# Optimization experiments

Measured on AMD Instinct MI355X. Metric: run time of the kernel, lower is better.

Reference implementation:

```python
import jax, jax.numpy as jnp
import numpy as np

HEADS = 16
KEY = 64          # key_size == size_per_head
NEG = 1e10


def setup_inputs() -> dict:
    key = jax.random.key(0)
    k1, k2, k3, k4, k5, k6 = jax.random.split(key, 6)
    B, S, D = 2, 2048, 1024
    scale = 1.0 / np.sqrt(D).astype(np.float32)
    return {
        "q": jax.random.normal(k1, (B, S, D), jnp.float32),
        "k": jax.random.normal(k2, (B, S, D), jnp.float32),
        "v": jax.random.normal(k3, (B, S, D), jnp.float32),
        "Wq": jax.random.normal(k4, (D, HEADS * KEY), jnp.float32) * scale,
        "Wk": jax.random.normal(k5, (D, HEADS * KEY), jnp.float32) * scale,
        "Wv": jax.random.normal(k6, (D, HEADS * KEY), jnp.float32) * scale,
    }


def reference(q, k, v, Wq, Wk, Wv):
    B, Sq, _ = q.shape
    Skv = k.shape[1]
    # projections (no bias), split heads: (B, S, H*Dh) -> (B, H, S, Dh)
    qw = (q @ Wq).reshape(B, Sq, HEADS, KEY).transpose(0, 2, 1, 3)
    kw = (k @ Wk).reshape(B, Skv, HEADS, KEY).transpose(0, 2, 1, 3)
    vw = (v @ Wv).reshape(B, Skv, HEADS, KEY).transpose(0, 2, 1, 3)
    inv_sqrt_d = jnp.asarray(1.0 / np.sqrt(KEY), dtype=qw.dtype)
    a = jnp.einsum("bhqd,bhkd->bhqk", qw, kw) * inv_sqrt_d  # (B,H,Sq,Skv)
    # mask_right=True: causal additive mask a - (1 - tril)*1e10
    causal = jnp.tril(jnp.ones((Sq, Skv), dtype=a.dtype))
    a = a - (1.0 - causal) * jnp.asarray(NEG, dtype=a.dtype)
    a = jax.nn.softmax(a, axis=-1)
    o = jnp.einsum("bhqk,bhkd->bhqd", a, vw)  # (B,H,Sq,Dh)
    o = o.transpose(0, 2, 1, 3).reshape(B, Sq, HEADS * KEY)
    return o
```

## Files before the change

kernel.cpp:

```cpp
#include <hip/hip_runtime.h>
#include <hip/hip_bf16.h>

#define HEADS 16
#define KEY   64
#define BB    2
#define SS    2048
#define DD    1024
#define NCOL  1024

typedef __attribute__((ext_vector_type(8))) short bf16x8;
typedef __attribute__((ext_vector_type(4))) float f32x4;
typedef __attribute__((ext_vector_type(8))) unsigned short u16x8;

typedef const __attribute__((address_space(1))) void* gas_ptr;
typedef __attribute__((address_space(3))) void* las_ptr;

__device__ __forceinline__ void gload_lds16(const void* g, void* l) {
  __builtin_amdgcn_global_load_lds((gas_ptr)g, (las_ptr)l, 16, 0, 0);
}

__device__ __forceinline__ unsigned short f2bf(float f) {
  unsigned u = __builtin_bit_cast(unsigned, f);
  u = (u + 0x7FFFu + ((u >> 16) & 1u)) >> 16;
  return (unsigned short)u;
}

__device__ __forceinline__ float bf2f(unsigned short u) {
  return __builtin_bit_cast(float, (unsigned)u << 16);
}

__device__ __forceinline__ unsigned cvtpk(float lo, float hi) {
  unsigned r;
  asm("v_cvt_pk_bf16_f32 %0, %1, %2" : "=v"(r) : "v"(lo), "v"(hi));
  return r;
}

__device__ __forceinline__ f32x4 mfma_bf16(bf16x8 a, bf16x8 b, f32x4 c) {
  return __builtin_amdgcn_mfma_f32_16x16x32_bf16(a, b, c, 0, 0, 0);
}

__global__ __launch_bounds__(256) void cvt_bf16(const float* __restrict__ in,
                                                unsigned short* __restrict__ out,
                                                int n8) {
  int i = blockIdx.x * blockDim.x + threadIdx.x;
  if (i >= n8) return;
  const float4* p = reinterpret_cast<const float4*>(in) + (size_t)i * 2;
  float4 a = p[0], b = p[1];
  u16x8 o;
  o[0] = f2bf(a.x); o[1] = f2bf(a.y); o[2] = f2bf(a.z); o[3] = f2bf(a.w);
  o[4] = f2bf(b.x); o[5] = f2bf(b.y); o[6] = f2bf(b.z); o[7] = f2bf(b.w);
  reinterpret_cast<u16x8*>(out)[i] = o;
}

__global__ __launch_bounds__(1024) void trw(const float* __restrict__ W0,
                                            const float* __restrict__ W1,
                                            const float* __restrict__ W2,
                                            unsigned short* __restrict__ T0,
                                            unsigned short* __restrict__ T1,
                                            unsigned short* __restrict__ T2) {
  const float* W = blockIdx.z == 0 ? W0 : (blockIdx.z == 1 ? W1 : W2);
  unsigned short* T = blockIdx.z == 0 ? T0 : (blockIdx.z == 1 ? T1 : T2);
  __shared__ float tile[32][33];
  int tx = threadIdx.x, ty = threadIdx.y;
  tile[ty][tx] = W[(size_t)(blockIdx.y * 32 + ty) * DD + blockIdx.x * 32 + tx];
  __syncthreads();
  T[(size_t)(blockIdx.x * 32 + ty) * DD + blockIdx.y * 32 + tx] = f2bf(tile[tx][ty]);
}

__global__ __launch_bounds__(1024) void trv(const unsigned short* __restrict__ vwp,
                                            unsigned short* __restrict__ vt) {
  __shared__ unsigned short tile[32][33];
  const int bh = blockIdx.z, b = bh >> 4, h = bh & 15;
  const int s0 = blockIdx.x * 32, d0 = blockIdx.y * 32;
  const int tx = threadIdx.x, ty = threadIdx.y;
  tile[ty][tx] = vwp[(size_t)(b * SS + s0 + ty) * NCOL + h * KEY + d0 + tx];
  __syncthreads();
  vt[((size_t)bh * KEY + d0 + ty) * SS + s0 + tx] = tile[tx][ty];
}

__global__ __launch_bounds__(256) void gemm_proj(
    const unsigned short* __restrict__ X0, const unsigned short* __restrict__ X1,
    const unsigned short* __restrict__ X2,
    const unsigned short* __restrict__ W0, const unsigned short* __restrict__ W1,
    const unsigned short* __restrict__ W2,
    unsigned short* __restrict__ O0, unsigned short* __restrict__ O1,
    unsigned short* __restrict__ O2) {
  const unsigned short* X; const unsigned short* WT; unsigned short* O;
  if (blockIdx.z == 0)      { X = X0; WT = W0; O = O0; }
  else if (blockIdx.z == 1) { X = X1; WT = W1; O = O1; }
  else                      { X = X2; WT = W2; O = O2; }

  __shared__ __align__(16) unsigned short As[128 * 32];
  __shared__ __align__(16) unsigned short Bs[128 * 32];

  const int tid = threadIdx.x;
  const int w = tid >> 6, l = tid & 63;
  const int m0 = blockIdx.x * 128, n0 = blockIdx.y * 128;
  const int wm = (w >> 1) * 64, wn = (w & 1) * 64;
  const int g = l >> 4, c = l & 15;

  const int srow = tid >> 2;
  const int scol = (tid & 3) * 8;

  f32x4 acc[4][4] = {};

  for (int k0 = 0; k0 < DD; k0 += 32) {
#pragma unroll
    for (int i = 0; i < 2; ++i) {
      gload_lds16(X + (size_t)(m0 + i * 64 + srow) * DD + k0 + scol,
                  (char*)As + i * 4096 + w * 1024);
      gload_lds16(WT + (size_t)(n0 + i * 64 + srow) * DD + k0 + scol,
                  (char*)Bs + i * 4096 + w * 1024);
    }
    __syncthreads();
    bf16x8 af[4], bfr[4];
    const int kb = g * 8;
#pragma unroll
    for (int mi = 0; mi < 4; mi++)
      af[mi] = *reinterpret_cast<const bf16x8*>(&As[(wm + mi * 16 + c) * 32 + kb]);
#pragma unroll
    for (int ni = 0; ni < 4; ni++)
      bfr[ni] = *reinterpret_cast<const bf16x8*>(&Bs[(wn + ni * 16 + c) * 32 + kb]);
#pragma unroll
    for (int mi = 0; mi < 4; mi++)
#pragma unroll
      for (int ni = 0; ni < 4; ni++)
        acc[mi][ni] = mfma_bf16(af[mi], bfr[ni], acc[mi][ni]);
    __syncthreads();
  }

#pragma unroll
  for (int mi = 0; mi < 4; mi++)
#pragma unroll
    for (int ni = 0; ni < 4; ni++)
#pragma unroll
      for (int r = 0; r < 4; r++) {
        int row = m0 + wm + mi * 16 + g * 4 + r;
        int col = n0 + wn + ni * 16 + c;
        O[(size_t)row * NCOL + col] = f2bf(acc[mi][ni][r]);
      }
}

__global__ __launch_bounds__(256) void attn(const unsigned short* __restrict__ qw,
                                            const unsigned short* __restrict__ kw,
                                            const unsigned short* __restrict__ vt,
                                            unsigned short* __restrict__ opart,
                                            float* __restrict__ mlb,
                                            float* __restrict__ out) {
  __shared__ __align__(16) char smem[40960];
  char* KsRaw = smem;
  char* VsRaw = smem + 16384;
  unsigned short* Pl = (unsigned short*)(smem + 32768);
  float* Osc = (float*)smem;

  const int tid = threadIdx.x, w = tid >> 6, l = tid & 63;
  const int g = l >> 4, c = l & 15;
  const int x = blockIdx.x, h = blockIdx.y, b = blockIdx.z;

  int qt, ci, nchunks;
  if (x < 8)       { qt = x;                ci = 0;            nchunks = 1; }
  else if (x < 24) { qt = 8 + ((x - 8) >> 1);  ci = (x - 8) & 1;  nchunks = 2; }
  else if (x < 48) { qt = 16 + (x - 24) / 3;   ci = (x - 24) % 3; nchunks = 3; }
  else             { qt = 24 + ((x - 48) >> 2); ci = (x - 48) & 3; nchunks = 4; }
  const int nt = qt + 1;
  const int t_begin = ci * 8;
  const int t_end = min(t_begin + 8, nt);
  const int q0 = qt * 64;
  const int cid = (b * HEADS + h) * 80 + x;

  const int qrow = q0 + w * 16 + c;
  const size_t qbase = ((size_t)(b * SS) + qrow) * NCOL + h * KEY;
  bf16x8 qf[2];
  qf[0] = *reinterpret_cast<const bf16x8*>(qw + qbase + g * 8);
  qf[1] = *reinterpret_cast<const bf16x8*>(qw + qbase + g * 8 + 32);

  f32x4 oacc[4] = {};
  float m = -1e30f, lsum = 0.f;

  const int krow = w * 8 + (l >> 3);
  const int kcsw = 8 * ((l & 7) ^ (l >> 3));
  const size_t kbase = (size_t)(b * SS) * NCOL + h * KEY;
  const size_t vbase = (size_t)(b * HEADS + h) * KEY * SS;

  {
    const int kv0 = t_begin * 64;
#pragma unroll
    for (int j = 0; j < 2; ++j) {
      gload_lds16(kw + kbase + (size_t)(kv0 + j * 32 + krow) * NCOL + kcsw,
                  KsRaw + j * 4096 + w * 1024);
      gload_lds16(vt + vbase + (size_t)(j * 32 + krow) * SS + kv0 + kcsw,
                  VsRaw + j * 4096 + w * 1024);
    }
  }
  __syncthreads();

  const float SC = 0.125f * 1.44269504089f;
  unsigned short* Pw = Pl + w * 1024;
  int cur = 0;
  for (int it = t_begin; it < t_end; ++it) {
    if (it + 1 < t_end) {
      const int kv1 = (it + 1) * 64, nx = cur ^ 1;
#pragma unroll
      for (int j = 0; j < 2; ++j) {
        gload_lds16(kw + kbase + (size_t)(kv1 + j * 32 + krow) * NCOL + kcsw,
                    KsRaw + nx * 8192 + j * 4096 + w * 1024);
        gload_lds16(vt + vbase + (size_t)(j * 32 + krow) * SS + kv1 + kcsw,
                    VsRaw + nx * 8192 + j * 4096 + w * 1024);
      }
    }
    const unsigned short* Kc = (const unsigned short*)(KsRaw + cur * 8192);
    const unsigned short* Vc = (const unsigned short*)(VsRaw + cur * 8192);

    f32x4 sacc[4] = {};
    __builtin_amdgcn_s_setprio(1);
#pragma unroll
    for (int t = 0; t < 4; t++)
#pragma unroll
      for (int ks = 0; ks < 2; ks++) {
        const int off = ((g | (ks << 2)) ^ (c & 7)) << 3;
        bf16x8 kf = *reinterpret_cast<const bf16x8*>(&Kc[(t * 16 + c) * 64 + off]);
        sacc[t] = mfma_bf16(kf, qf[ks], sacc[t]);
      }
    __builtin_amdgcn_s_setprio(0);

    float p[4][4], pm = -3.0e38f;
    const bool dg = (it == nt - 1);
#pragma unroll
    for (int t = 0; t < 4; t++)
#pragma unroll
      for (int r = 0; r < 4; r++) {
        float s = sacc[t][r] * SC;
        if (dg && (it * 64 + 16 * t + 4 * g + r > qrow)) s = -3.0e38f;
        p[t][r] = s;
        pm = fmaxf(pm, s);
      }
    pm = fmaxf(pm, __shfl_xor(pm, 16));
    pm = fmaxf(pm, __shfl_xor(pm, 32));
    if (__ballot(pm > m)) {
      float mn = fmaxf(m, pm);
      float al = exp2f(m - mn);
      m = mn; lsum *= al;
#pragma unroll
      for (int t = 0; t < 4; t++) oacc[t] *= al;
    }
    float rs = 0.f;
#pragma unroll
    for (int t = 0; t < 4; t++)
#pragma unroll
      for (int r = 0; r < 4; r++) {
        float e = exp2f(p[t][r] - m);
        p[t][r] = e;
        rs += e;
      }
    rs += __shfl_xor(rs, 16);
    rs += __shfl_xor(rs, 32);
    lsum += rs;

#pragma unroll
    for (int t = 0; t < 4; t++)
#pragma unroll
      for (int rr = 0; rr < 2; rr++) {
        unsigned pk = cvtpk(p[t][2 * rr], p[t][2 * rr + 1]);
        int col = 16 * t + 4 * g + 2 * rr;
        *reinterpret_cast<unsigned*>(&Pw[c * 64 + (col ^ ((c & 7) << 3))]) = pk;
      }
    bf16x8 pf[2];
#pragma unroll
    for (int ks = 0; ks < 2; ks++)
      pf[ks] = *reinterpret_cast<const bf16x8*>(
          &Pw[c * 64 + (((g | (ks << 2)) ^ (c & 7)) << 3)]);

    __builtin_amdgcn_s_setprio(1);
#pragma unroll
    for (int t = 0; t < 4; t++)
#pragma unroll
      for (int ks = 0; ks < 2; ks++) {
        const int off = ((g | (ks << 2)) ^ (c & 7)) << 3;
        bf16x8 vf = *reinterpret_cast<const bf16x8*>(&Vc[(t * 16 + c) * 64 + off]);
        oacc[t] = mfma_bf16(vf, pf[ks], oacc[t]);
      }
    __builtin_amdgcn_s_setprio(0);
    __syncthreads();
    cur ^= 1;
  }

  const float inv = (nchunks == 1) ? 1.0f / lsum : 1.0f;
#pragma unroll
  for (int t = 0; t < 4; t++)
#pragma unroll
    for (int rr = 0; rr < 2; rr++) {
      float2 v2 = make_float2(oacc[t][2 * rr] * inv, oacc[t][2 * rr + 1] * inv);
      *reinterpret_cast<float2*>(&Osc[(w * 16 + c) * 72 + 16 * t + 4 * g + 2 * rr]) = v2;
    }
  if (nchunks > 1 && l < 16) {
    float* mlp = mlb + (size_t)cid * 128 + w * 16 + c;
    mlp[0] = m;
    mlp[64] = lsum;
  }
  __syncthreads();

  const int row = tid >> 2, sg = (tid & 3) << 4;
  if (nchunks == 1) {
    float* op = out + ((size_t)(b * SS) + q0 + row) * NCOL + h * KEY + sg;
#pragma unroll
    for (int kk = 0; kk < 4; kk++)
      reinterpret_cast<float4*>(op)[kk] =
          *reinterpret_cast<const float4*>(&Osc[row * 72 + sg + kk * 4]);
  } else {
    unsigned* pp = reinterpret_cast<unsigned*>(opart + (size_t)cid * 4096 + row * 64 + sg);
#pragma unroll
    for (int e = 0; e < 8; e++)
      pp[e] = cvtpk(Osc[row * 72 + sg + 2 * e], Osc[row * 72 + sg + 2 * e + 1]);
  }
}

__global__ __launch_bounds__(256) void attn_reduce(const unsigned short* __restrict__ opart,
                                                   const float* __restrict__ mlb,
                                                   float* __restrict__ out) {
  const int qt = 8 + blockIdx.x, h = blockIdx.y, b = blockIdx.z;
  int base, nc;
  if (qt < 16)      { base = 8 + 2 * (qt - 8);   nc = 2; }
  else if (qt < 24) { base = 24 + 3 * (qt - 16); nc = 3; }
  else              { base = 48 + 4 * (qt - 24); nc = 4; }
  const int cid0 = (b * HEADS + h) * 80 + base;
  const int row = threadIdx.x >> 2, sg = (threadIdx.x & 3) << 4;

  float mv[4], lv[4], M = -1e30f;
#pragma unroll
  for (int i = 0; i < 4; i++)
    if (i < nc) {
      mv[i] = mlb[(size_t)(cid0 + i) * 128 + row];
      lv[i] = mlb[(size_t)(cid0 + i) * 128 + 64 + row];
      M = fmaxf(M, mv[i]);
    }
  float L = 0.f, acc[16];
#pragma unroll
  for (int e = 0; e < 16; e++) acc[e] = 0.f;
#pragma unroll
  for (int i = 0; i < 4; i++)
    if (i < nc) {
      float s = exp2f(mv[i] - M);
      L += s * lv[i];
      const u16x8* pp = reinterpret_cast<const u16x8*>(
          opart + (size_t)(cid0 + i) * 4096 + row * 64 + sg);
      u16x8 o0 = pp[0], o1 = pp[1];
#pragma unroll
      for (int e = 0; e < 8; e++) {
        acc[e]     += s * bf2f(o0[e]);
        acc[8 + e] += s * bf2f(o1[e]);
      }
    }
  const float inv = 1.0f / L;
  float* op = out + ((size_t)(b * SS) + qt * 64 + row) * NCOL + h * KEY + sg;
#pragma unroll
  for (int kk = 0; kk < 4; kk++) {
    float4 v;
    v.x = acc[4 * kk] * inv;     v.y = acc[4 * kk + 1] * inv;
    v.z = acc[4 * kk + 2] * inv; v.w = acc[4 * kk + 3] * inv;
    reinterpret_cast<float4*>(op)[kk] = v;
  }
}

extern "C" void kernel_launch(void* const* d_in, const int* in_sizes, int n_in,
                              void* d_out, int out_size, void* d_ws, size_t ws_size,
                              hipStream_t stream) {
  const float* q  = (const float*)d_in[0];
  const float* k  = (const float*)d_in[1];
  const float* v  = (const float*)d_in[2];
  const float* Wq = (const float*)d_in[3];
  const float* Wk = (const float*)d_in[4];
  const float* Wv = (const float*)d_in[5];
  float* out = (float*)d_out;

  unsigned short* ws  = (unsigned short*)d_ws;
  const size_t ACT = (size_t)4 * 1024 * 1024;
  const size_t WEL = (size_t)1024 * 1024;
  unsigned short* qbf = ws;
  unsigned short* kbf = qbf + ACT;
  unsigned short* vbf = kbf + ACT;
  unsigned short* WqT = vbf + ACT;
  unsigned short* WkT = WqT + WEL;
  unsigned short* WvT = WkT + WEL;
  unsigned short* qwp = WvT + WEL;
  unsigned short* kwp = qwp + ACT;
  unsigned short* vwp = kwp + ACT;
  unsigned short* vtb   = qbf;
  unsigned short* opart = kbf;
  float*          mlb   = (float*)WvT;

  cvt_bf16<<<2048, 256, 0, stream>>>(q, qbf, 524288);
  cvt_bf16<<<2048, 256, 0, stream>>>(k, kbf, 524288);
  cvt_bf16<<<2048, 256, 0, stream>>>(v, vbf, 524288);
  trw<<<dim3(32, 32, 3), dim3(32, 32), 0, stream>>>(Wq, Wk, Wv, WqT, WkT, WvT);
  gemm_proj<<<dim3(32, 8, 3), 256, 0, stream>>>(qbf, kbf, vbf, WqT, WkT, WvT,
                                                qwp, kwp, vwp);
  trv<<<dim3(64, 2, 32), dim3(32, 32), 0, stream>>>(vwp, vtb);
  attn<<<dim3(80, 16, 2), 256, 0, stream>>>(qwp, kwp, vtb, opart, mlb, out);
  attn_reduce<<<dim3(24, 16, 2), 256, 0, stream>>>(opart, mlb, out);
}
```

Measured before the change: 219.2 us.

## Fuse V transpose into projection GEMM, fold softmax scale, swizzle LDS, merge casts

```diff
diff --git a/kernel.cpp b/kernel.cpp
--- a/kernel.cpp
+++ b/kernel.cpp
@@ -39,11 +39,15 @@
   return __builtin_amdgcn_mfma_f32_16x16x32_bf16(a, b, c, 0, 0, 0);
 }
 
-__global__ __launch_bounds__(256) void cvt_bf16(const float* __restrict__ in,
-                                                unsigned short* __restrict__ out,
-                                                int n8) {
+__global__ __launch_bounds__(256) void cvt3(const float* __restrict__ q,
+                                            const float* __restrict__ k,
+                                            const float* __restrict__ v,
+                                            unsigned short* __restrict__ qo,
+                                            unsigned short* __restrict__ ko,
+                                            unsigned short* __restrict__ vo) {
+  const float* in = blockIdx.y == 0 ? q : (blockIdx.y == 1 ? k : v);
+  unsigned short* out = blockIdx.y == 0 ? qo : (blockIdx.y == 1 ? ko : vo);
   int i = blockIdx.x * blockDim.x + threadIdx.x;
-  if (i >= n8) return;
   const float4* p = reinterpret_cast<const float4*>(in) + (size_t)i * 2;
   float4 a = p[0], b = p[1];
   u16x8 o;
@@ -67,29 +71,10 @@
   T[(size_t)(blockIdx.x * 32 + ty) * DD + blockIdx.y * 32 + tx] = f2bf(tile[tx][ty]);
 }
 
-__global__ __launch_bounds__(1024) void trv(const unsigned short* __restrict__ vwp,
-                                            unsigned short* __restrict__ vt) {
-  __shared__ unsigned short tile[32][33];
-  const int bh = blockIdx.z, b = bh >> 4, h = bh & 15;
-  const int s0 = blockIdx.x * 32, d0 = blockIdx.y * 32;
-  const int tx = threadIdx.x, ty = threadIdx.y;
-  tile[ty][tx] = vwp[(size_t)(b * SS + s0 + ty) * NCOL + h * KEY + d0 + tx];
-  __syncthreads();
-  vt[((size_t)bh * KEY + d0 + ty) * SS + s0 + tx] = tile[tx][ty];
-}
-
-__global__ __launch_bounds__(256) void gemm_proj(
-    const unsigned short* __restrict__ X0, const unsigned short* __restrict__ X1,
-    const unsigned short* __restrict__ X2,
-    const unsigned short* __restrict__ W0, const unsigned short* __restrict__ W1,
-    const unsigned short* __restrict__ W2,
-    unsigned short* __restrict__ O0, unsigned short* __restrict__ O1,
-    unsigned short* __restrict__ O2) {
-  const unsigned short* X; const unsigned short* WT; unsigned short* O;
-  if (blockIdx.z == 0)      { X = X0; WT = W0; O = O0; }
-  else if (blockIdx.z == 1) { X = X1; WT = W1; O = O1; }
-  else                      { X = X2; WT = W2; O = O2; }
-
+template <int MODE>
+__global__ __launch_bounds__(256) void gemm_proj(const unsigned short* __restrict__ X,
+                                                 const unsigned short* __restrict__ WT,
+                                                 unsigned short* __restrict__ O) {
   __shared__ __align__(16) unsigned short As[128 * 32];
   __shared__ __align__(16) unsigned short Bs[128 * 32];
 
@@ -100,7 +85,8 @@
   const int g = l >> 4, c = l & 15;
 
   const int srow = tid >> 2;
-  const int scol = (tid & 3) * 8;
+  const int scol = 8 * ((tid & 3) ^ ((tid >> 3) & 3));
+  const int kb = ((g ^ ((c >> 1) & 3)) << 3);
 
   f32x4 acc[4][4] = {};
 
@@ -114,7 +100,6 @@
     }
     __syncthreads();
     bf16x8 af[4], bfr[4];
-    const int kb = g * 8;
 #pragma unroll
     for (int mi = 0; mi < 4; mi++)
       af[mi] = *reinterpret_cast<const bf16x8*>(&As[(wm + mi * 16 + c) * 32 + kb]);
@@ -124,21 +109,42 @@
 #pragma unroll
     for (int mi = 0; mi < 4; mi++)
 #pragma unroll
+      for (int ni = 0; ni < 4; ni++) {
+        if constexpr (MODE == 2)
+          acc[mi][ni] = mfma_bf16(bfr[ni], af[mi], acc[mi][ni]);
+        else
+          acc[mi][ni] = mfma_bf16(af[mi], bfr[ni], acc[mi][ni]);
+      }
+    __syncthreads();
+  }
+
+  if constexpr (MODE != 2) {
+    const float osc = (MODE == 0) ? 0.180336880f : 1.0f;
+#pragma unroll
+    for (int mi = 0; mi < 4; mi++)
+#pragma unroll
       for (int ni = 0; ni < 4; ni++)
-        acc[mi][ni] = mfma_bf16(af[mi], bfr[ni], acc[mi][ni]);
-    __syncthreads();
-  }
-
-#pragma unroll
-  for (int mi = 0; mi < 4; mi++)
-#pragma unroll
-    for (int ni = 0; ni < 4; ni++)
-#pragma unroll
-      for (int r = 0; r < 4; r++) {
-        int row = m0 + wm + mi * 16 + g * 4 + r;
-        int col = n0 + wn + ni * 16 + c;
-        O[(size_t)row * NCOL + col] = f2bf(acc[mi][ni][r]);
-      }
+#pragma unroll
+        for (int r = 0; r < 4; r++) {
+          int row = m0 + wm + mi * 16 + g * 4 + r;
+          int col = n0 + wn + ni * 16 + c;
+          O[(size_t)row * NCOL + col] = f2bf(acc[mi][ni][r] * osc);
+        }
+  } else {
+#pragma unroll
+    for (int mi = 0; mi < 4; mi++) {
+      const int mbase = m0 + wm + mi * 16;
+      const int bb_ = mbase >> 11;
+      const int s = (mbase & 2047) + c;
+#pragma unroll
+      for (int ni = 0; ni < 4; ni++)
+#pragma unroll
+        for (int r = 0; r < 4; r++) {
+          int n = n0 + wn + ni * 16 + g * 4 + r;
+          O[((size_t)(bb_ * 1024 + n) << 11) + s] = f2bf(acc[mi][ni][r]);
+        }
+    }
+  }
 }
 
 __global__ __launch_bounds__(256) void attn(const unsigned short* __restrict__ qw,
@@ -194,7 +200,6 @@
   }
   __syncthreads();
 
-  const float SC = 0.125f * 1.44269504089f;
   unsigned short* Pw = Pl + w * 1024;
   int cur = 0;
   for (int it = t_begin; it < t_end; ++it) {
@@ -223,35 +228,40 @@
       }
     __builtin_amdgcn_s_setprio(0);
 
-    float p[4][4], pm = -3.0e38f;
-    const bool dg = (it == nt - 1);
+    float p[4][4];
 #pragma unroll
     for (int t = 0; t < 4; t++)
 #pragma unroll
-      for (int r = 0; r < 4; r++) {
-        float s = sacc[t][r] * SC;
-        if (dg && (it * 64 + 16 * t + 4 * g + r > qrow)) s = -3.0e38f;
-        p[t][r] = s;
-        pm = fmaxf(pm, s);
-      }
+      for (int r = 0; r < 4; r++) p[t][r] = sacc[t][r];
+    if (it == nt - 1) {
+#pragma unroll
+      for (int t = 0; t < 4; t++)
+#pragma unroll
+        for (int r = 0; r < 4; r++)
+          if (it * 64 + 16 * t + 4 * g + r > qrow) p[t][r] = -3.0e38f;
+    }
+    float tm[4];
+#pragma unroll
+    for (int t = 0; t < 4; t++)
+      tm[t] = fmaxf(fmaxf(p[t][0], p[t][1]), fmaxf(p[t][2], p[t][3]));
+    float pm = fmaxf(fmaxf(tm[0], tm[1]), fmaxf(tm[2], tm[3]));
     pm = fmaxf(pm, __shfl_xor(pm, 16));
     pm = fmaxf(pm, __shfl_xor(pm, 32));
-    if (__ballot(pm > m)) {
+    if (__ballot(pm > m + 8.0f)) {
       float mn = fmaxf(m, pm);
       float al = exp2f(m - mn);
       m = mn; lsum *= al;
 #pragma unroll
       for (int t = 0; t < 4; t++) oacc[t] *= al;
     }
-    float rs = 0.f;
-#pragma unroll
-    for (int t = 0; t < 4; t++)
-#pragma unroll
-      for (int r = 0; r < 4; r++) {
-        float e = exp2f(p[t][r] - m);
-        p[t][r] = e;
-        rs += e;
-      }
+    float ts[4];
+#pragma unroll
+    for (int t = 0; t < 4; t++) {
+#pragma unroll
+      for (int r = 0; r < 4; r++) p[t][r] = exp2f(p[t][r] - m);
+      ts[t] = (p[t][0] + p[t][1]) + (p[t][2] + p[t][3]);
+    }
+    float rs = (ts[0] + ts[1]) + (ts[2] + ts[3]);
     rs += __shfl_xor(rs, 16);
     rs += __shfl_xor(rs, 32);
     lsum += rs;
@@ -383,18 +393,15 @@
   unsigned short* WvT = WkT + WEL;
   unsigned short* qwp = WvT + WEL;
   unsigned short* kwp = qwp + ACT;
-  unsigned short* vwp = kwp + ACT;
-  unsigned short* vtb   = qbf;
+  unsigned short* vt  = kwp + ACT;
   unsigned short* opart = kbf;
   float*          mlb   = (float*)WvT;
 
-  cvt_bf16<<<2048, 256, 0, stream>>>(q, qbf, 524288);
-  cvt_bf16<<<2048, 256, 0, stream>>>(k, kbf, 524288);
-  cvt_bf16<<<2048, 256, 0, stream>>>(v, vbf, 524288);
+  cvt3<<<dim3(2048, 3), 256, 0, stream>>>(q, k, v, qbf, kbf, vbf);
   trw<<<dim3(32, 32, 3), dim3(32, 32), 0, stream>>>(Wq, Wk, Wv, WqT, WkT, WvT);
-  gemm_proj<<<dim3(32, 8, 3), 256, 0, stream>>>(qbf, kbf, vbf, WqT, WkT, WvT,
-                                                qwp, kwp, vwp);
-  trv<<<dim3(64, 2, 32), dim3(32, 32), 0, stream>>>(vwp, vtb);
-  attn<<<dim3(80, 16, 2), 256, 0, stream>>>(qwp, kwp, vtb, opart, mlb, out);
+  gemm_proj<0><<<dim3(32, 8), 256, 0, stream>>>(qbf, WqT, qwp);
+  gemm_proj<1><<<dim3(32, 8), 256, 0, stream>>>(kbf, WkT, kwp);
+  gemm_proj<2><<<dim3(32, 8), 256, 0, stream>>>(vbf, WvT, vt);
+  attn<<<dim3(80, 16, 2), 256, 0, stream>>>(qwp, kwp, vt, opart, mlb, out);
   attn_reduce<<<dim3(24, 16, 2), 256, 0, stream>>>(opart, mlb, out);
 }
```

New measurement: 227.9 us. 4.0% more time.
